# Performance work log

Hardware: AMD Instinct MI355X
Metric: run time of the kernel (lower is better)

Reference implementation:

```python
import jax, jax.numpy as jnp
import numpy as np

B, S, E, H = 2, 2048, 1024, 16
D = E // H  # head_dim = 64


def setup_inputs() -> dict:
    key = jax.random.key(0)
    ks = jax.random.split(key, 6)
    scale = 1.0 / np.sqrt(E)
    query = jax.random.normal(ks[0], (B, S, E), dtype=jnp.float32)
    key_t = jax.random.normal(ks[1], (B, S, E), dtype=jnp.float32)
    # causal mask: True where future positions should be masked
    attention_mask = jnp.triu(jnp.ones((S, S), dtype=jnp.bool_), k=1)
    wq = jax.random.normal(ks[2], (E, E), dtype=jnp.float32) * scale
    wk = jax.random.normal(ks[3], (E, E), dtype=jnp.float32) * scale
    wv = jax.random.normal(ks[4], (E, E), dtype=jnp.float32) * scale
    wo = jax.random.normal(ks[5], (E, E), dtype=jnp.float32) * scale
    return {"query": query, "key": key_t, "attention_mask": attention_mask,
            "wq": wq, "wk": wk, "wv": wv, "wo": wo}


def _split_heads(x):
    # (B, S, E) -> (B, H, S, D)
    return x.reshape(B, S, H, D).transpose(0, 2, 1, 3)


def reference(query, key, attention_mask, wq, wk, wv, wo):
    # self-attention (encoder_decoder_attention=False): k, v from query
    q = _split_heads(query @ wq.T)
    k = _split_heads(query @ wk.T)
    v = _split_heads(query @ wv.T)
    scores = jnp.einsum('bhqd,bhkd->bhqk', q, k) / np.sqrt(D)
    # causal mask broadcast (1,1,S,S)
    scores = jnp.where(attention_mask[None, None, :, :], -jnp.inf, scores)
    attn_weights = jax.nn.softmax(scores, axis=-1)
    # drop_out = 0.0, so dropout is identity
    attn_out = jnp.einsum('bhqk,bhkd->bhqd', attn_weights, v)
    attn_out = attn_out.transpose(0, 2, 1, 3).reshape(B, S, E)
    attn_out = attn_out @ wo.T
    return attn_out, attn_weights
```

## Files before the change

kernel.cpp:

```cpp
#include <hip/hip_runtime.h>
#include <hip/hip_bf16.h>
#include <cstdint>

#define S_LEN 2048
#define EMB 1024
#define NHEAD 16
#define HDIM 64
#define NB 2
#define MTOT (NB * S_LEN)

typedef __attribute__((ext_vector_type(8))) __bf16 bf16x8;
typedef __attribute__((ext_vector_type(8))) unsigned short us8;
typedef __attribute__((ext_vector_type(4))) unsigned short us4;
typedef __attribute__((ext_vector_type(4))) float f32x4;

__device__ __forceinline__ unsigned short f2b(float f) {
  unsigned int u = __float_as_uint(f);
  u = (u + 0x7FFFu + ((u >> 16) & 1u)) >> 16;
  return (unsigned short)u;
}
__device__ __forceinline__ unsigned short f2b_tr(float f) {
  return (unsigned short)(__float_as_uint(f) >> 16);
}
__device__ __forceinline__ bf16x8 ld8(const unsigned short* p) {
  return __builtin_bit_cast(bf16x8, *(const us8*)p);
}
__device__ __forceinline__ void gload16(const void* g, void* l) {
  __builtin_amdgcn_global_load_lds(
      (const __attribute__((address_space(1))) unsigned int*)g,
      (__attribute__((address_space(3))) unsigned int*)l, 16, 0, 0);
}

__global__ void conv_b16(const float* __restrict__ in,
                         unsigned short* __restrict__ out, int n4) {
  int stride = gridDim.x * blockDim.x;
  for (int i = blockIdx.x * blockDim.x + threadIdx.x; i < n4; i += stride) {
    float4 v = reinterpret_cast<const float4*>(in)[i];
    us4 o;
    o[0] = f2b(v.x); o[1] = f2b(v.y); o[2] = f2b(v.z); o[3] = f2b(v.w);
    reinterpret_cast<us4*>(out)[i] = o;
  }
}

__global__ void conv4_b16(const float* __restrict__ a, const float* __restrict__ b,
                          const float* __restrict__ c, const float* __restrict__ d,
                          unsigned short* __restrict__ out) {
  int i = blockIdx.x * blockDim.x + threadIdx.x;
  int sel = i >> 18, j = i & 262143;
  const float* s = sel == 0 ? a : sel == 1 ? b : sel == 2 ? c : d;
  float4 v = reinterpret_cast<const float4*>(s)[j];
  us4 o;
  o[0] = f2b(v.x); o[1] = f2b(v.y); o[2] = f2b(v.z); o[3] = f2b(v.w);
  reinterpret_cast<us4*>(out)[i] = o;
}

__global__ __launch_bounds__(256)
void vtrans(const unsigned short* __restrict__ V, unsigned short* __restrict__ VT) {
  __shared__ unsigned short Vs[64][72];
  const int s0 = blockIdx.x * 64;
  const int bh = blockIdx.y, b = bh >> 4, h = bh & 15;
  const unsigned short* Vb = V + (size_t)b * S_LEN * EMB + h * HDIM;
  const int t = threadIdx.x;
  {
    int row = t >> 2, c0 = (t & 3) * 16;
    const unsigned short* src = Vb + (size_t)(s0 + row) * EMB + c0;
    *(us8*)&Vs[row][c0] = *(const us8*)src;
    *(us8*)&Vs[row][c0 + 8] = *(const us8*)(src + 8);
  }
  __syncthreads();
  int d = t >> 2, sc = (t & 3) * 16;
  us8 o0, o1;
#pragma unroll
  for (int j = 0; j < 8; ++j) { o0[j] = Vs[sc + j][d]; o1[j] = Vs[sc + 8 + j][d]; }
  unsigned short* dst = VT + ((size_t)bh * HDIM + d) * S_LEN + s0 + sc;
  *(us8*)dst = o0;
  *(us8*)(dst + 8) = o1;
}

template <typename OT>
__global__ __launch_bounds__(256)
void gemm_bt(const unsigned short* __restrict__ A,
             const unsigned short* __restrict__ Wb,
             OT* __restrict__ Cb) {
  __shared__ unsigned short As[128 * 32];
  __shared__ unsigned short Bs[128 * 32];
  const int t = threadIdx.x;
  const int w = t >> 6, l = t & 63;
  const int m0 = blockIdx.x * 128;
  const int n0g = blockIdx.y * 128;
  const int wsel = n0g >> 10;
  const int n0 = n0g & 1023;
  const unsigned short* W = Wb + (size_t)wsel * ((size_t)EMB * EMB);
  OT* C = Cb + (size_t)wsel * ((size_t)MTOT * EMB);
  const int wr = (w >> 1) * 64, wc = (w & 1) * 64;
  const int fr = l & 15, fk = (l >> 4) * 8;
  const f32x4 fz = {0.f, 0.f, 0.f, 0.f};
  f32x4 acc[4][4];
  for (int i = 0; i < 4; i++)
    for (int j = 0; j < 4; j++) acc[i][j] = fz;
  const int srow = t >> 2, scol = (t & 3) * 8;
  const unsigned short* Ar = A + (size_t)(m0 + srow) * EMB + scol;
  const unsigned short* Wr = W + (size_t)(n0 + srow) * EMB + scol;
  unsigned short* lA = &As[t * 8];
  unsigned short* lB = &Bs[t * 8];
  for (int k0 = 0; k0 < EMB; k0 += 32) {
    gload16(Ar + k0, lA);
    gload16(Ar + (size_t)64 * EMB + k0, lA + 64 * 32);
    gload16(Wr + k0, lB);
    gload16(Wr + (size_t)64 * EMB + k0, lB + 64 * 32);
    __syncthreads();
    bf16x8 af[4], bg[4];
#pragma unroll
    for (int i = 0; i < 4; i++) {
      af[i] = ld8(&As[(wr + i * 16 + fr) * 32 + fk]);
      bg[i] = ld8(&Bs[(wc + i * 16 + fr) * 32 + fk]);
    }
#pragma unroll
    for (int i = 0; i < 4; i++)
#pragma unroll
      for (int j = 0; j < 4; j++)
        acc[i][j] = __builtin_amdgcn_mfma_f32_16x16x32_bf16(af[i], bg[j], acc[i][j], 0, 0, 0);
    __syncthreads();
  }
  const int cr = (l >> 4) * 4, cc = l & 15;
#pragma unroll
  for (int i = 0; i < 4; i++)
#pragma unroll
    for (int j = 0; j < 4; j++) {
      int m = m0 + wr + i * 16 + cr;
      int n = n0 + wc + j * 16 + cc;
      OT* dst = C + (size_t)m * EMB + n;
#pragma unroll
      for (int r = 0; r < 4; r++) {
        if constexpr (sizeof(OT) == 2)
          dst[(size_t)r * EMB] = f2b(acc[i][j][r]);
        else
          dst[(size_t)r * EMB] = acc[i][j][r];
      }
    }
}

__global__ __launch_bounds__(256, 2)
void attn_fwd(const unsigned short* __restrict__ Q,
              const unsigned short* __restrict__ K,
              const unsigned short* __restrict__ VT,
              unsigned short* __restrict__ AO,
              float* __restrict__ WT) {
  __shared__ __align__(16) unsigned char smem[9216 * 2 + 18432 * 2];
  unsigned short* Ks = (unsigned short*)smem;
  unsigned short* Vt = (unsigned short*)(smem + 9216);
  float* PfA = (float*)(smem + 18432);
  float* PfB = (float*)(smem + 18432 + 18432);
  unsigned short* QsA = (unsigned short*)PfA;
  unsigned short* QsB = (unsigned short*)PfB;
  unsigned short* OlA = (unsigned short*)PfA;
  unsigned short* OlB = (unsigned short*)PfB;

  const int t = threadIdx.x, w = t >> 6, l = t & 63;
  const int bh = blockIdx.x, b = bh >> 4, h = bh & 15;
  const int p = blockIdx.y;
  const int qA = p, qB = (S_LEN / 64 - 1) - p;
  const int ntA = qA + 1, ntB = qB + 1;
  const unsigned short* Qb = Q + (size_t)b * S_LEN * EMB + h * HDIM;
  const unsigned short* Kb = K + (size_t)b * S_LEN * EMB + h * HDIM;
  const unsigned short* VTb = VT + (size_t)bh * HDIM * S_LEN;
  const int fr = l & 15, fk = (l >> 4) * 8;
  const int rg = (l >> 4) * 4;
  const int qrowA = qA * 64 + w * 16 + rg;
  const int qrowB = qB * 64 + w * 16 + rg;
  const f32x4 fz = {0.f, 0.f, 0.f, 0.f};

  {
    int row = t >> 2, c0 = (t & 3) * 16;
    const unsigned short* sA = Qb + (size_t)(qA * 64 + row) * EMB + c0;
    const unsigned short* sB = Qb + (size_t)(qB * 64 + row) * EMB + c0;
    *(us8*)&QsA[row * 72 + c0] = *(const us8*)sA;
    *(us8*)&QsA[row * 72 + c0 + 8] = *(const us8*)(sA + 8);
    *(us8*)&QsB[row * 72 + c0] = *(const us8*)sB;
    *(us8*)&QsB[row * 72 + c0 + 8] = *(const us8*)(sB + 8);
  }
  __syncthreads();
  bf16x8 qaA0 = ld8(&QsA[(w * 16 + fr) * 72 + fk]);
  bf16x8 qaA1 = ld8(&QsA[(w * 16 + fr) * 72 + 32 + fk]);
  bf16x8 qaB0 = ld8(&QsB[(w * 16 + fr) * 72 + fk]);
  bf16x8 qaB1 = ld8(&QsB[(w * 16 + fr) * 72 + 32 + fk]);

  float mrA[4], lrA[4], mrB[4], lrB[4];
#pragma unroll
  for (int r = 0; r < 4; r++) { mrA[r] = mrB[r] = -1e30f; lrA[r] = lrB[r] = 0.f; }

  for (int it = 0; it < ntB; ++it) {
    const int kc = it * 64;
#pragma unroll
    for (int i = 0; i < 2; ++i) {
      int c = t + 256 * i;
      int row = c >> 3, c0 = (c & 7) * 8;
      *(us8*)&Ks[row * 72 + c0] = *(const us8*)(Kb + (size_t)(kc + row) * EMB + c0);
    }
    __syncthreads();
#pragma unroll
    for (int half = 0; half < 2; ++half) {
      if (half == 0 && it >= ntA) continue;
      const bf16x8 q0 = half ? qaB0 : qaA0, q1 = half ? qaB1 : qaA1;
      const int qrow = half ? qrowB : qrowA;
      const bool diag = half ? (it == ntB - 1) : (it == ntA - 1);
      float* mr = half ? mrB : mrA;
      float* lr = half ? lrB : lrA;
      float sc[4][4];
#pragma unroll
      for (int c = 0; c < 4; ++c) {
        f32x4 dd = fz;
        dd = __builtin_amdgcn_mfma_f32_16x16x32_bf16(q0, ld8(&Ks[(c * 16 + fr) * 72 + fk]), dd, 0, 0, 0);
        dd = __builtin_amdgcn_mfma_f32_16x16x32_bf16(q1, ld8(&Ks[(c * 16 + fr) * 72 + 32 + fk]), dd, 0, 0, 0);
        int ki = kc + c * 16 + fr;
#pragma unroll
        for (int r = 0; r < 4; ++r) {
          float s = dd[r] * 0.125f;
          if (diag && ki > qrow + r) s = -1e30f;
          sc[c][r] = s;
        }
      }
#pragma unroll
      for (int r = 0; r < 4; ++r) {
        float cm = fmaxf(fmaxf(sc[0][r], sc[1][r]), fmaxf(sc[2][r], sc[3][r]));
        float mn = fmaxf(mr[r], cm);
        lr[r] = lr[r] * __expf(mr[r] - mn) + __expf(sc[0][r] - mn) + __expf(sc[1][r] - mn)
              + __expf(sc[2][r] - mn) + __expf(sc[3][r] - mn);
        mr[r] = mn;
      }
    }
    __syncthreads();
  }
#pragma unroll
  for (int r = 0; r < 4; ++r) {
    float mA = mrA[r], lA = lrA[r], mB = mrB[r], lB = lrB[r];
    for (int s = 1; s < 16; s <<= 1) {
      float om = __shfl_xor(mA, s, 64), ol = __shfl_xor(lA, s, 64);
      float mn = fmaxf(mA, om);
      lA = lA * __expf(mA - mn) + ol * __expf(om - mn);
      mA = mn;
      om = __shfl_xor(mB, s, 64); ol = __shfl_xor(lB, s, 64);
      mn = fmaxf(mB, om);
      lB = lB * __expf(mB - mn) + ol * __expf(om - mn);
      mB = mn;
    }
    mrA[r] = mA; lrA[r] = 1.0f / lA;
    mrB[r] = mB; lrB[r] = 1.0f / lB;
  }

  f32x4 accA[4], accB[4];
#pragma unroll
  for (int i = 0; i < 4; i++) { accA[i] = fz; accB[i] = fz; }
  float* PfAw = PfA + w * (16 * 72);
  float* PfBw = PfB + w * (16 * 72);
  for (int it = 0; it < ntB; ++it) {
    const int kc = it * 64;
#pragma unroll
    for (int i = 0; i < 2; ++i) {
      int c = t + 256 * i;
      int row = c >> 3, c0 = (c & 7) * 8;
      *(us8*)&Ks[row * 72 + c0] = *(const us8*)(Kb + (size_t)(kc + row) * EMB + c0);
      *(us8*)&Vt[row * 72 + c0] = *(const us8*)(VTb + (size_t)row * S_LEN + kc + c0);
    }
    __syncthreads();
#pragma unroll
    for (int half = 0; half < 2; ++half) {
      if (half == 0 && it >= ntA) continue;
      const bf16x8 q0 = half ? qaB0 : qaA0, q1 = half ? qaB1 : qaA1;
      const int qrow = half ? qrowB : qrowA;
      const bool diag = half ? (it == ntB - 1) : (it == ntA - 1);
      const float* mr = half ? mrB : mrA;
      const float* lr = half ? lrB : lrA;
      float* Pfw = half ? PfBw : PfAw;
#pragma unroll
      for (int c = 0; c < 4; ++c) {
        f32x4 dd = fz;
        dd = __builtin_amdgcn_mfma_f32_16x16x32_bf16(q0, ld8(&Ks[(c * 16 + fr) * 72 + fk]), dd, 0, 0, 0);
        dd = __builtin_amdgcn_mfma_f32_16x16x32_bf16(q1, ld8(&Ks[(c * 16 + fr) * 72 + 32 + fk]), dd, 0, 0, 0);
        int ki = kc + c * 16 + fr;
#pragma unroll
        for (int r = 0; r < 4; ++r) {
          float s = dd[r] * 0.125f;
          if (diag && ki > qrow + r) s = -1e30f;
          Pfw[(rg + r) * 72 + c * 16 + fr] = __expf(s - mr[r]) * lr[r];
        }
      }
    }
    __syncthreads();
#pragma unroll
    for (int half = 0; half < 2; ++half) {
      if (half == 0 && it >= ntA) continue;
      const float* Pfw = half ? PfBw : PfAw;
      f32x4* acc = half ? accB : accA;
      const int qq = half ? qB : qA;
#pragma unroll
      for (int ks = 0; ks < 2; ++ks) {
        f32x4 p0 = *(const f32x4*)&Pfw[fr * 72 + ks * 32 + fk];
        f32x4 p1 = *(const f32x4*)&Pfw[fr * 72 + ks * 32 + fk + 4];
        us8 uu;
#pragma unroll
        for (int j = 0; j < 4; ++j) { uu[j] = f2b_tr(p0[j]); uu[j + 4] = f2b_tr(p1[j]); }
        bf16x8 pa = __builtin_bit_cast(bf16x8, uu);
#pragma unroll
        for (int dt = 0; dt < 4; ++dt) {
          bf16x8 vb = ld8(&Vt[(dt * 16 + fr) * 72 + ks * 32 + fk]);
          acc[dt] = __builtin_amdgcn_mfma_f32_16x16x32_bf16(pa, vb, acc[dt], 0, 0, 0);
        }
      }
#pragma unroll
      for (int s4 = 0; s4 < 4; ++s4) {
        int rowl = s4 * 4 + (l >> 4);
        f32x4 v = *(const f32x4*)&Pfw[rowl * 72 + (l & 15) * 4];
        *(f32x4*)&WT[((size_t)bh * S_LEN + qq * 64 + w * 16 + rowl) * S_LEN + kc + (l & 15) * 4] = v;
      }
    }
    __syncthreads();
  }

#pragma unroll
  for (int half = 0; half < 2; ++half) {
    const int qq = half ? qB : qA;
    const int kend = (half ? ntB : ntA) * 64;
#pragma unroll
    for (int s4 = 0; s4 < 4; ++s4) {
      int rowl = s4 * 4 + (l >> 4);
      size_t base = ((size_t)bh * S_LEN + qq * 64 + w * 16 + rowl) * S_LEN;
      for (int k = kend + (l & 15) * 4; k < S_LEN; k += 64)
        *(f32x4*)&WT[base + k] = fz;
    }
  }
#pragma unroll
  for (int dt = 0; dt < 4; ++dt)
#pragma unroll
    for (int r = 0; r < 4; ++r) {
      OlA[(w * 16 + rg + r) * 72 + dt * 16 + fr] = f2b(accA[dt][r]);
      OlB[(w * 16 + rg + r) * 72 + dt * 16 + fr] = f2b(accB[dt][r]);
    }
  __syncthreads();
  {
    int rowl = l >> 2, d0 = (l & 3) * 16;
    us8 a0 = *(const us8*)&OlA[(w * 16 + rowl) * 72 + d0];
    us8 a1 = *(const us8*)&OlA[(w * 16 + rowl) * 72 + d0 + 8];
    unsigned short* dA = AO + (size_t)(b * S_LEN + qA * 64 + w * 16 + rowl) * EMB + h * HDIM + d0;
    *(us8*)dA = a0;
    *(us8*)(dA + 8) = a1;
    us8 b0 = *(const us8*)&OlB[(w * 16 + rowl) * 72 + d0];
    us8 b1 = *(const us8*)&OlB[(w * 16 + rowl) * 72 + d0 + 8];
    unsigned short* dB = AO + (size_t)(b * S_LEN + qB * 64 + w * 16 + rowl) * EMB + h * HDIM + d0;
    *(us8*)dB = b0;
    *(us8*)(dB + 8) = b1;
  }
}

extern "C" void kernel_launch(void* const* d_in, const int* in_sizes, int n_in,
                              void* d_out, int out_size, void* d_ws, size_t ws_size,
                              hipStream_t stream) {
  const float* query = (const float*)d_in[0];
  const float* wq = (const float*)d_in[3];
  const float* wk = (const float*)d_in[4];
  const float* wv = (const float*)d_in[5];
  const float* wo = (const float*)d_in[6];

  float* out0 = (float*)d_out;
  float* wout = out0 + (size_t)MTOT * EMB;

  unsigned short* xb  = (unsigned short*)d_ws;
  unsigned short* wqb = xb + (size_t)MTOT * EMB;
  unsigned short* wkb = wqb + (size_t)EMB * EMB;
  unsigned short* wvb = wkb + (size_t)EMB * EMB;
  unsigned short* wob = wvb + (size_t)EMB * EMB;
  unsigned short* qb  = wob + (size_t)EMB * EMB;
  unsigned short* kb  = qb + (size_t)MTOT * EMB;
  unsigned short* vb  = kb + (size_t)MTOT * EMB;
  unsigned short* ab  = vb + (size_t)MTOT * EMB;
  unsigned short* vtg = xb;

  conv_b16<<<dim3(2048), dim3(256), 0, stream>>>(query, xb, MTOT * EMB / 4);
  conv4_b16<<<dim3(4096), dim3(256), 0, stream>>>(wq, wk, wv, wo, wqb);

  gemm_bt<unsigned short><<<dim3(MTOT / 128, 24), dim3(256), 0, stream>>>(xb, wqb, qb);

  vtrans<<<dim3(S_LEN / 64, NB * NHEAD), dim3(256), 0, stream>>>(vb, vtg);

  attn_fwd<<<dim3(NB * NHEAD, S_LEN / 128), dim3(256), 0, stream>>>(qb, kb, vtg, ab, wout);

  gemm_bt<float><<<dim3(MTOT / 128, 8), dim3(256), 0, stream>>>(ab, wob, out0);
}
```

Measured before the change: 234.6 us.

## Store attention probabilities as bf16 in LDS and prefetch K/V tiles through registers

The per-wave probability tile moves from fp32 to bf16 in shared memory, which halves the kernel's LDS footprint. Launch bounds rise from two to three blocks per CU to use the freed space. K and V tiles are now loaded into registers one iteration ahead, so global loads overlap with the previous tile's compute. In exchange, the written attention weights are rounded to bf16 before being widened back to fp32, which lowers their precision, and the extra prefetch registers compete with the higher occupancy target.

```diff
diff --git a/kernel.cpp b/kernel.cpp
--- a/kernel.cpp
+++ b/kernel.cpp
@@ -19,8 +19,8 @@
   u = (u + 0x7FFFu + ((u >> 16) & 1u)) >> 16;
   return (unsigned short)u;
 }
-__device__ __forceinline__ unsigned short f2b_tr(float f) {
-  return (unsigned short)(__float_as_uint(f) >> 16);
+__device__ __forceinline__ float b2f(unsigned short u) {
+  return __uint_as_float((unsigned int)u << 16);
 }
 __device__ __forceinline__ bf16x8 ld8(const unsigned short* p) {
   return __builtin_bit_cast(bf16x8, *(const us8*)p);
@@ -140,21 +140,21 @@
     }
 }
 
-__global__ __launch_bounds__(256, 2)
+__global__ __launch_bounds__(256, 3)
 void attn_fwd(const unsigned short* __restrict__ Q,
               const unsigned short* __restrict__ K,
               const unsigned short* __restrict__ VT,
               unsigned short* __restrict__ AO,
               float* __restrict__ WT) {
-  __shared__ __align__(16) unsigned char smem[9216 * 2 + 18432 * 2];
-  unsigned short* Ks = (unsigned short*)smem;
-  unsigned short* Vt = (unsigned short*)(smem + 9216);
-  float* PfA = (float*)(smem + 18432);
-  float* PfB = (float*)(smem + 18432 + 18432);
-  unsigned short* QsA = (unsigned short*)PfA;
-  unsigned short* QsB = (unsigned short*)PfB;
-  unsigned short* OlA = (unsigned short*)PfA;
-  unsigned short* OlB = (unsigned short*)PfB;
+  __shared__ __align__(16) unsigned char smem[9216 * 4];
+  unsigned short* Ks  = (unsigned short*)smem;
+  unsigned short* Vt  = (unsigned short*)(smem + 9216);
+  unsigned short* PsA = (unsigned short*)(smem + 18432);
+  unsigned short* PsB = (unsigned short*)(smem + 27648);
+  unsigned short* QsA = PsA;
+  unsigned short* QsB = PsB;
+  unsigned short* OlA = PsA;
+  unsigned short* OlB = PsB;
 
   const int t = threadIdx.x, w = t >> 6, l = t & 63;
   const int bh = blockIdx.x, b = bh >> 4, h = bh & 15;
@@ -169,6 +169,7 @@
   const int qrowA = qA * 64 + w * 16 + rg;
   const int qrowB = qB * 64 + w * 16 + rg;
   const f32x4 fz = {0.f, 0.f, 0.f, 0.f};
+  const int srow = t >> 3, scol = (t & 7) * 8;
 
   {
     int row = t >> 2, c0 = (t & 3) * 16;
@@ -189,15 +190,19 @@
 #pragma unroll
   for (int r = 0; r < 4; r++) { mrA[r] = mrB[r] = -1e30f; lrA[r] = lrB[r] = 0.f; }
 
+  us8 k0r = *(const us8*)(Kb + (size_t)srow * EMB + scol);
+  us8 k1r = *(const us8*)(Kb + (size_t)(srow + 32) * EMB + scol);
   for (int it = 0; it < ntB; ++it) {
+    *(us8*)&Ks[srow * 72 + scol] = k0r;
+    *(us8*)&Ks[(srow + 32) * 72 + scol] = k1r;
+    us8 k0n, k1n;
+    if (it + 1 < ntB) {
+      const unsigned short* kn = Kb + (size_t)((it + 1) * 64) * EMB;
+      k0n = *(const us8*)(kn + (size_t)srow * EMB + scol);
+      k1n = *(const us8*)(kn + (size_t)(srow + 32) * EMB + scol);
+    }
+    __syncthreads();
     const int kc = it * 64;
-#pragma unroll
-    for (int i = 0; i < 2; ++i) {
-      int c = t + 256 * i;
-      int row = c >> 3, c0 = (c & 7) * 8;
-      *(us8*)&Ks[row * 72 + c0] = *(const us8*)(Kb + (size_t)(kc + row) * EMB + c0);
-    }
-    __syncthreads();
 #pragma unroll
     for (int half = 0; half < 2; ++half) {
       if (half == 0 && it >= ntA) continue;
@@ -230,6 +235,7 @@
       }
     }
     __syncthreads();
+    k0r = k0n; k1r = k1n;
   }
 #pragma unroll
   for (int r = 0; r < 4; ++r) {
@@ -251,18 +257,29 @@
   f32x4 accA[4], accB[4];
 #pragma unroll
   for (int i = 0; i < 4; i++) { accA[i] = fz; accB[i] = fz; }
-  float* PfAw = PfA + w * (16 * 72);
-  float* PfBw = PfB + w * (16 * 72);
+  unsigned short* PsAw = PsA + w * (16 * 72);
+  unsigned short* PsBw = PsB + w * (16 * 72);
+  us8 v0r, v1r;
+  k0r = *(const us8*)(Kb + (size_t)srow * EMB + scol);
+  k1r = *(const us8*)(Kb + (size_t)(srow + 32) * EMB + scol);
+  v0r = *(const us8*)(VTb + (size_t)srow * S_LEN + scol);
+  v1r = *(const us8*)(VTb + (size_t)(srow + 32) * S_LEN + scol);
   for (int it = 0; it < ntB; ++it) {
+    *(us8*)&Ks[srow * 72 + scol] = k0r;
+    *(us8*)&Ks[(srow + 32) * 72 + scol] = k1r;
+    *(us8*)&Vt[srow * 72 + scol] = v0r;
+    *(us8*)&Vt[(srow + 32) * 72 + scol] = v1r;
+    us8 k0n, k1n, v0n, v1n;
+    if (it + 1 < ntB) {
+      const int kc1 = (it + 1) * 64;
+      const unsigned short* kn = Kb + (size_t)kc1 * EMB;
+      k0n = *(const us8*)(kn + (size_t)srow * EMB + scol);
+      k1n = *(const us8*)(kn + (size_t)(srow + 32) * EMB + scol);
+      v0n = *(const us8*)(VTb + (size_t)srow * S_LEN + kc1 + scol);
+      v1n = *(const us8*)(VTb + (size_t)(srow + 32) * S_LEN + kc1 + scol);
+    }
+    __syncthreads();
     const int kc = it * 64;
-#pragma unroll
-    for (int i = 0; i < 2; ++i) {
-      int c = t + 256 * i;
-      int row = c >> 3, c0 = (c & 7) * 8;
-      *(us8*)&Ks[row * 72 + c0] = *(const us8*)(Kb + (size_t)(kc + row) * EMB + c0);
-      *(us8*)&Vt[row * 72 + c0] = *(const us8*)(VTb + (size_t)row * S_LEN + kc + c0);
-    }
-    __syncthreads();
 #pragma unroll
     for (int half = 0; half < 2; ++half) {
       if (half == 0 && it >= ntA) continue;
@@ -271,7 +288,7 @@
       const bool diag = half ? (it == ntB - 1) : (it == ntA - 1);
       const float* mr = half ? mrB : mrA;
       const float* lr = half ? lrB : lrA;
-      float* Pfw = half ? PfBw : PfAw;
+      unsigned short* Pw = half ? PsBw : PsAw;
 #pragma unroll
       for (int c = 0; c < 4; ++c) {
         f32x4 dd = fz;
@@ -282,7 +299,7 @@
         for (int r = 0; r < 4; ++r) {
           float s = dd[r] * 0.125f;
           if (diag && ki > qrow + r) s = -1e30f;
-          Pfw[(rg + r) * 72 + c * 16 + fr] = __expf(s - mr[r]) * lr[r];
+          Pw[(rg + r) * 72 + c * 16 + fr] = f2b(__expf(s - mr[r]) * lr[r]);
         }
       }
     }
@@ -290,17 +307,12 @@
 #pragma unroll
     for (int half = 0; half < 2; ++half) {
       if (half == 0 && it >= ntA) continue;
-      const float* Pfw = half ? PfBw : PfAw;
+      const unsigned short* Pw = half ? PsBw : PsAw;
       f32x4* acc = half ? accB : accA;
       const int qq = half ? qB : qA;
 #pragma unroll
       for (int ks = 0; ks < 2; ++ks) {
-        f32x4 p0 = *(const f32x4*)&Pfw[fr * 72 + ks * 32 + fk];
-        f32x4 p1 = *(const f32x4*)&Pfw[fr * 72 + ks * 32 + fk + 4];
-        us8 uu;
-#pragma unroll
-        for (int j = 0; j < 4; ++j) { uu[j] = f2b_tr(p0[j]); uu[j + 4] = f2b_tr(p1[j]); }
-        bf16x8 pa = __builtin_bit_cast(bf16x8, uu);
+        bf16x8 pa = ld8(&Pw[fr * 72 + ks * 32 + fk]);
 #pragma unroll
         for (int dt = 0; dt < 4; ++dt) {
           bf16x8 vb = ld8(&Vt[(dt * 16 + fr) * 72 + ks * 32 + fk]);
@@ -310,11 +322,15 @@
 #pragma unroll
       for (int s4 = 0; s4 < 4; ++s4) {
         int rowl = s4 * 4 + (l >> 4);
-        f32x4 v = *(const f32x4*)&Pfw[rowl * 72 + (l & 15) * 4];
+        us4 pv = *(const us4*)&Pw[rowl * 72 + (l & 15) * 4];
+        f32x4 v;
+#pragma unroll
+        for (int j = 0; j < 4; ++j) v[j] = b2f(pv[j]);
         *(f32x4*)&WT[((size_t)bh * S_LEN + qq * 64 + w * 16 + rowl) * S_LEN + kc + (l & 15) * 4] = v;
       }
     }
     __syncthreads();
+    k0r = k0n; k1r = k1n; v0r = v0n; v1r = v1n;
   }
 
 #pragma unroll
```

Result: no change. 231.0 us (-1.5%).
